# Performance work log

Measured on AMD Instinct MI355X. Metric: run time of the kernel, lower is better.

Reference implementation:

```python
import jax, jax.numpy as jnp
import numpy as np

F32 = jnp.float32
G_VEC = jnp.array([0.0, 0.0, -9.80665], dtype=F32)
# KITTI-style filter parameters (process / initial covariances)
COV_OMEGA = 1e-3; COV_ACC = 1e-2; COV_B_OMEGA = 6e-9; COV_B_ACC = 2e-4
COV_ROT_C_I = 1e-9; COV_T_C_I = 1e-9
COV_ROT0 = 1e-3; COV_V0 = 1e-1; COV_B_OMEGA0 = 1e-1; COV_B_ACC0 = 1e-1
COV_ROT_C_I0 = 1e-6; COV_T_C_I0 = 1e-5
Q_DIAG = jnp.array([COV_OMEGA]*3 + [COV_ACC]*3 + [COV_B_OMEGA]*3 + [COV_B_ACC]*3
                   + [COV_ROT_C_I]*3 + [COV_T_C_I]*3, dtype=F32)


def skew(x):
    z = jnp.zeros((), x.dtype)
    return jnp.stack([jnp.stack([z, -x[2], x[1]]),
                      jnp.stack([x[2], z, -x[0]]),
                      jnp.stack([-x[1], x[0], z])])


def so3exp(phi):
    I = jnp.eye(3, dtype=phi.dtype)
    angle = jnp.linalg.norm(phi)
    small = angle < 1e-8
    a = jnp.where(small, 1.0, angle)
    S = skew(phi)
    R = I + (jnp.sin(a) / a) * S + ((1.0 - jnp.cos(a)) / (a * a)) * (S @ S)
    return jnp.where(small, I + S, R)


def sen3exp(xi):
    phi = xi[:3]
    I = jnp.eye(3, dtype=xi.dtype)
    angle = jnp.linalg.norm(phi)
    small = angle < 1e-8
    a = jnp.where(small, 1.0, angle)
    S = skew(phi)
    SS = S @ S
    Rot = jnp.where(small, I + S,
                    I + (jnp.sin(a) / a) * S + ((1.0 - jnp.cos(a)) / (a * a)) * SS)
    J = jnp.where(small, I + 0.5 * S,
                  I + ((1.0 - jnp.cos(a)) / (a * a)) * S + ((a - jnp.sin(a)) / (a ** 3)) * SS)
    x = J @ xi[3:9].reshape(2, 3).T  # (3,2): columns dv, dp
    return Rot, x


def from_rpy(roll, pitch, yaw):
    c, s = jnp.cos, jnp.sin
    z = jnp.zeros((), roll.dtype); o = jnp.ones((), roll.dtype)
    Rz = jnp.stack([jnp.stack([c(yaw), -s(yaw), z]), jnp.stack([s(yaw), c(yaw), z]), jnp.stack([z, z, o])])
    Ry = jnp.stack([jnp.stack([c(pitch), z, s(pitch)]), jnp.stack([z, o, z]), jnp.stack([-s(pitch), z, c(pitch)])])
    Rx = jnp.stack([jnp.stack([o, z, z]), jnp.stack([z, c(roll), -s(roll)]), jnp.stack([z, s(roll), c(roll)])])
    return Rz @ Ry @ Rx


def _run(t, u, measurements_covs, v_mes, ang0, w_init):
    I3 = jnp.eye(3, dtype=F32)
    IdP = jnp.eye(21, dtype=F32)
    Q = jnp.diag(Q_DIAG)
    dt = t[1:] - t[:-1]
    # InitProcessCovNet.init_cov: beta = 10 ** tanh(W @ 1)
    beta = 10.0 ** jnp.tanh(w_init)
    P0 = jnp.zeros((21, 21), F32)
    I2 = jnp.eye(2, dtype=F32)
    P0 = P0.at[:2, :2].set(COV_ROT0 * beta[0] * I2)
    P0 = P0.at[3:5, 3:5].set(COV_V0 * beta[1] * I2)
    P0 = P0.at[9:12, 9:12].set(COV_B_OMEGA0 * beta[2] * I3)
    P0 = P0.at[12:15, 12:15].set(COV_B_ACC0 * beta[3] * I3)
    P0 = P0.at[15:18, 15:18].set(COV_ROT_C_I0 * beta[4] * I3)
    P0 = P0.at[18:21, 18:21].set(COV_T_C_I0 * beta[5] * I3)
    Rot0 = from_rpy(ang0[0], ang0[1], ang0[2])
    z3 = jnp.zeros(3, F32)
    state0 = (Rot0, v_mes[0], z3, z3, z3, I3, z3, P0)

    def step(carry, inp):
        Rot_p, v_p, p_p, bo_p, ba_p, Rci_p, tci_p, P = carry
        u_i, dt_i, mc_i = inp
        # ---- propagate ----
        acc = Rot_p @ (u_i[3:6] - ba_p) + G_VEC
        v = v_p + acc * dt_i
        p = p_p + v_p * dt_i + 0.5 * acc * dt_i * dt_i
        omega = (u_i[:3] - bo_p) * dt_i
        Rot = Rot_p @ so3exp(omega)
        # ---- covariance propagation ----
        vsr = skew(v_p) @ Rot_p
        psr = skew(p_p) @ Rot_p
        F = jnp.zeros((21, 21), F32)
        F = F.at[3:6, :3].set(skew(G_VEC))
        F = F.at[6:9, 3:6].set(I3)
        F = F.at[3:6, 12:15].set(-Rot_p)
        F = F.at[:3, 9:12].set(-Rot_p)
        F = F.at[3:6, 9:12].set(-vsr)
        F = F.at[6:9, 9:12].set(-psr)
        Gm = jnp.zeros((21, 18), F32)
        Gm = Gm.at[:3, :3].set(Rot_p)
        Gm = Gm.at[3:6, 3:6].set(Rot_p)
        Gm = Gm.at[3:6, :3].set(vsr)
        Gm = Gm.at[6:9, :3].set(psr)
        Gm = Gm.at[9:12, 6:9].set(I3)
        Gm = Gm.at[12:15, 9:12].set(I3)
        Gm = Gm.at[15:18, 12:15].set(I3)
        Gm = Gm.at[18:21, 15:18].set(I3)
        F = F * dt_i
        Gm = Gm * dt_i
        F2 = F @ F
        Phi = IdP + F + 0.5 * F2 + (F2 @ F) / 6.0
        P = Phi @ (P + Gm @ Q @ Gm.T) @ Phi.T
        # ---- update (zero lateral/vertical body velocity pseudo-measurement) ----
        Rot_body = Rot @ Rci_p
        v_imu = Rot.T @ v
        om = u_i[:3] - bo_p
        v_body = Rci_p.T @ v_imu + skew(tci_p) @ om
        Omega = skew(om)
        H_v_imu = Rci_p.T @ skew(v_imu)
        H_t = skew(tci_p)
        H = jnp.zeros((2, 21), F32)
        H = H.at[:, 3:6].set(Rot_body.T[1:])
        H = H.at[:, 15:18].set(H_v_imu[1:])
        H = H.at[:, 9:12].set(H_t[1:])
        H = H.at[:, 18:21].set(-Omega[1:])
        r = -v_body[1:]
        Rm = jnp.diag(mc_i)
        S = H @ P @ H.T + Rm
        K = jnp.linalg.solve(S, (P @ H.T).T).T  # (21,2)
        dx = K @ r
        dR, dxi = sen3exp(dx[:9])
        Rot_u = dR @ Rot
        v_u = dR @ v + dxi[:, 0]
        p_u = dR @ p + dxi[:, 1]
        bo_u = bo_p + dx[9:12]
        ba_u = ba_p + dx[12:15]
        Rci_u = so3exp(dx[15:18]) @ Rci_p
        tci_u = tci_p + dx[18:21]
        I_KH = IdP - K @ H
        P_u = I_KH @ P @ I_KH.T + K @ Rm @ K.T
        P_u = 0.5 * (P_u + P_u.T)
        new = (Rot_u, v_u, p_u, bo_u, ba_u, Rci_u, tci_u, P_u)
        return new, (Rot_u, v_u, p_u, bo_u, ba_u, Rci_u, tci_u)

    xs = (u[1:], dt, measurements_covs[1:])
    _, traj = jax.lax.scan(step, state0, xs)
    cat = lambda x0, xs_: jnp.concatenate([x0[None], xs_], axis=0)
    Rot = cat(Rot0, traj[0]); v = cat(state0[1], traj[1]); p = cat(state0[2], traj[2])
    bo = cat(state0[3], traj[3]); ba = cat(state0[4], traj[4])
    Rci = cat(I3, traj[5]); tci = cat(state0[6], traj[6])
    n = Rot.shape[0]
    # pack (Rot, v, p, b_omega, b_acc, Rot_c_i, t_c_i) -> [N, 30]
    return jnp.concatenate([Rot.reshape(n, 9), v, p, bo, ba, Rci.reshape(n, 9), tci], axis=1)


def setup_inputs() -> dict:
    key = jax.random.key(0)
    k1, k2, k3, k4, k5, k6 = jax.random.split(key, 6)
    N = 5000
    t = jnp.arange(N, dtype=F32) * 0.01  # 100 Hz IMU timestamps
    u = 0.1 * jax.random.normal(k1, (N, 6), dtype=F32)
    u = u.at[:, 5].add(9.80665)  # accel z ~ gravity
    measurements_covs = 0.5 * jax.random.uniform(k2, (N, 2), dtype=F32) + 0.1
    v_mes = jax.random.normal(k3, (N, 3), dtype=F32)
    p_mes = jax.random.normal(k4, (N, 3), dtype=F32)
    ang0 = 0.1 * jax.random.normal(k5, (3,), dtype=F32)
    w_init = 0.1 * jax.random.normal(k6, (6,), dtype=F32)
    return {"t": t, "u": u, "measurements_covs": measurements_covs,
            "v_mes": v_mes, "p_mes": p_mes, "ang0": ang0, "w_init": w_init, "N": N}


def reference(t, u, measurements_covs, v_mes, p_mes, ang0, w_init, N):
    # p_mes is accepted (as in run()) but unused: p[0] stays zero in init_run.
    return _run(t, u, measurements_covs, v_mes, ang0, w_init)
```

## Files before the change

### kernel.cpp

```cpp
#include <hip/hip_runtime.h>
#include <math.h>

#define GRV 9.80665f

__device__ __forceinline__ void so3coeffs(float a2, float* c1, float* c2, float* c3){
  if (a2 < 2.5e-3f){
    float a4 = a2*a2;
    *c1 = 1.f      - a2*(1.f/6.f)   + a4*(1.f/120.f);
    *c2 = 0.5f     - a2*(1.f/24.f)  + a4*(1.f/720.f);
    *c3 = (1.f/6.f)- a2*(1.f/120.f) + a4*(1.f/5040.f);
  } else {
    float a = sqrtf(a2);
    float sa = sinf(a), ca = cosf(a);
    *c1 = sa/a; *c2 = (1.f-ca)/a2; *c3 = (a-sa)/(a2*a);
  }
}

__device__ __forceinline__ void so3exp_u(float p0, float p1, float p2, float* R){
  float a2 = p0*p0+p1*p1+p2*p2;
  float c1,c2,c3; so3coeffs(a2,&c1,&c2,&c3);
  R[0]=1.f+c2*(p0*p0-a2); R[4]=1.f+c2*(p1*p1-a2); R[8]=1.f+c2*(p2*p2-a2);
  R[1]=-c1*p2+c2*p0*p1;   R[3]= c1*p2+c2*p0*p1;
  R[2]= c1*p1+c2*p0*p2;   R[6]=-c1*p1+c2*p0*p2;
  R[5]=-c1*p0+c2*p1*p2;   R[7]= c1*p0+c2*p1*p2;
}

__device__ __forceinline__ void mat3mul_u(const float* A, const float* B, float* C){
  #pragma unroll
  for (int r=0;r<3;r++)
    #pragma unroll
    for (int c=0;c<3;c++)
      C[r*3+c] = A[r*3]*B[c] + A[r*3+1]*B[3+c] + A[r*3+2]*B[6+c];
}

__device__ __forceinline__ void col_update(float* a, const float* R_, const float* n13,
                                           const float* n23, float dtv, float hdt2,
                                           float Gdt, float Ghdt2){
  float nb[9];
  #pragma unroll
  for (int jb=0;jb<3;jb++)
    nb[jb] = a[jb] - dtv*(R_[jb*3]*a[9]+R_[jb*3+1]*a[10]+R_[jb*3+2]*a[11]);
  #pragma unroll
  for (int r=0;r<3;r++){
    float s = a[3+r];
    if (r==0) s += Gdt*a[1];
    if (r==1) s -= Gdt*a[0];
    s += n13[r*3]*a[9]+n13[r*3+1]*a[10]+n13[r*3+2]*a[11];
    s -= dtv*(R_[r*3]*a[12]+R_[r*3+1]*a[13]+R_[r*3+2]*a[14]);
    nb[3+r]=s;
  }
  #pragma unroll
  for (int r=0;r<3;r++){
    float s = a[6+r];
    if (r==0) s += Ghdt2*a[1];
    if (r==1) s -= Ghdt2*a[0];
    s += dtv*a[3+r];
    s += n23[r*3]*a[9]+n23[r*3+1]*a[10]+n23[r*3+2]*a[11];
    s -= hdt2*(R_[r*3]*a[12]+R_[r*3+1]*a[13]+R_[r*3+2]*a[14]);
    nb[6+r]=s;
  }
  #pragma unroll
  for (int k=0;k<9;k++) a[k]=nb[k];
}

#define SEL9(e0,e1,e2,e3,e4,e5,e6,e7,e8) \
  (lane==0?(e0):lane==1?(e1):lane==2?(e2):lane==3?(e3):lane==4?(e4):lane==5?(e5):lane==6?(e6):lane==7?(e7):(e8))

__global__ __launch_bounds__(64)
void iekf_kernel(const float* __restrict__ t, const float* __restrict__ u,
                 const float* __restrict__ mcov, const float* __restrict__ vmes,
                 const float* __restrict__ ang0, const float* __restrict__ winit,
                 float* __restrict__ out, int N)
{
  const int lane = threadIdx.x;

  __shared__ float TP1[21*24];
  __shared__ float TP2[21*24];
  __shared__ float PH[44];
  __shared__ float stG[36];

  float R_[9], v_[3], p_[3], bo_[3], ba_[3], Rci_[9], tci_[3];
  float creg[21];

  float beta[6];
  #pragma unroll
  for (int k=0;k<6;k++) beta[k] = powf(10.f, tanhf(winit[k]));
  {
    float cr=cosf(ang0[0]), sr=sinf(ang0[0]);
    float cp=cosf(ang0[1]), sp=sinf(ang0[1]);
    float cy=cosf(ang0[2]), sy=sinf(ang0[2]);
    float Rz[9]={cy,-sy,0.f, sy,cy,0.f, 0.f,0.f,1.f};
    float Ry[9]={cp,0.f,sp, 0.f,1.f,0.f, -sp,0.f,cp};
    float Rx[9]={1.f,0.f,0.f, 0.f,cr,-sr, 0.f,sr,cr};
    float T1m[9]; mat3mul_u(Rz,Ry,T1m); mat3mul_u(T1m,Rx,R_);
  }
  v_[0]=vmes[0]; v_[1]=vmes[1]; v_[2]=vmes[2];
  #pragma unroll
  for (int k=0;k<3;k++){ p_[k]=0.f; bo_[k]=0.f; ba_[k]=0.f; tci_[k]=0.f; }
  #pragma unroll
  for (int k=0;k<9;k++) Rci_[k] = (k%4==0)?1.f:0.f;

  {
    float dl = (lane==0||lane==1)? 1e-3f*beta[0]
             : (lane==3||lane==4)? 0.1f*beta[1]
             : (lane>=9&&lane<12)? 0.1f*beta[2]
             : (lane>=12&&lane<15)? 0.1f*beta[3]
             : (lane>=15&&lane<18)? 1e-6f*beta[4]
             : (lane>=18&&lane<21)? 1e-5f*beta[5] : 0.f;
    #pragma unroll
    for (int j=0;j<21;j++) creg[j] = (j==lane)? dl : 0.f;
  }

  if (lane==0){
    ((float4*)stG)[0] = make_float4(R_[0],R_[1],R_[2],R_[3]);
    ((float4*)stG)[1] = make_float4(R_[4],R_[5],R_[6],R_[7]);
    ((float4*)stG)[2] = make_float4(R_[8],v_[0],v_[1],v_[2]);
    ((float4*)stG)[3] = make_float4(p_[0],p_[1],p_[2],bo_[0]);
    ((float4*)stG)[4] = make_float4(bo_[1],bo_[2],ba_[0],ba_[1]);
    ((float4*)stG)[5] = make_float4(ba_[2],Rci_[0],Rci_[1],Rci_[2]);
    ((float4*)stG)[6] = make_float4(Rci_[3],Rci_[4],Rci_[5],Rci_[6]);
    ((float4*)stG)[7] = make_float4(Rci_[7],Rci_[8],tci_[0],tci_[1]);
    ((float4*)stG)[8] = make_float4(tci_[2],0.f,0.f,0.f);
  }

  float t_nm1 = t[0];
  float t_n   = (N>1)? t[1] : t[0];
  float mc0   = (N>1)? mcov[2] : 0.f;
  float mc1   = (N>1)? mcov[3] : 0.f;
  float u6[6] = {0,0,0,0,0,0};
  if (N>1){
    #pragma unroll
    for (int k=0;k<6;k++) u6[k]=u[6+k];
  }

  for (int n=1; n<N; n++){
    const float dtv = t_n - t_nm1;
    const float dt2 = dtv*dtv;
    const float hdt2 = 0.5f*dt2;
    const float sdt3 = dt2*dtv*(1.f/6.f);
    const float Gdt = GRV*dtv;
    const float Ghdt2 = GRV*hdt2;

    if (lane<33) out[(size_t)(n-1)*33 + lane] = stG[lane];

    if (lane<21){
      float4* rp = (float4*)&TP1[lane*24];
      rp[0]=make_float4(creg[0],creg[1],creg[2],creg[3]);
      rp[1]=make_float4(creg[4],creg[5],creg[6],creg[7]);
      rp[2]=make_float4(creg[8],creg[9],creg[10],creg[11]);
      rp[3]=make_float4(creg[12],creg[13],creg[14],creg[15]);
      rp[4]=make_float4(creg[16],creg[17],creg[18],creg[19]);
      TP1[lane*24+20]=creg[20];
    }

    float vsr[9], psr[9], n13[9], n23[9];
    #pragma unroll
    for (int c=0;c<3;c++){
      vsr[c]   = v_[1]*R_[6+c] - v_[2]*R_[3+c];
      vsr[3+c] = v_[2]*R_[c]   - v_[0]*R_[6+c];
      vsr[6+c] = v_[0]*R_[3+c] - v_[1]*R_[c];
      psr[c]   = p_[1]*R_[6+c] - p_[2]*R_[3+c];
      psr[3+c] = p_[2]*R_[c]   - p_[0]*R_[6+c];
      psr[6+c] = p_[0]*R_[3+c] - p_[1]*R_[c];
    }
    #pragma unroll
    for (int c=0;c<3;c++){
      float sg0 =  GRV*R_[3+c];
      float sg1 = -GRV*R_[c];
      n13[c]   = -dtv*vsr[c]   - hdt2*sg0;
      n13[3+c] = -dtv*vsr[3+c] - hdt2*sg1;
      n13[6+c] = -dtv*vsr[6+c];
      n23[c]   = -dtv*psr[c]   - hdt2*vsr[c]   - sdt3*sg0;
      n23[3+c] = -dtv*psr[3+c] - hdt2*vsr[3+c] - sdt3*sg1;
      n23[6+c] = -dtv*psr[6+c] - hdt2*vsr[6+c];
    }

    float Rn[9], vnp[3], pnp[3];
    {
      float ub0=u6[3]-ba_[0], ub1=u6[4]-ba_[1], ub2=u6[5]-ba_[2];
      float ac0=R_[0]*ub0+R_[1]*ub1+R_[2]*ub2;
      float ac1=R_[3]*ub0+R_[4]*ub1+R_[5]*ub2;
      float ac2=R_[6]*ub0+R_[7]*ub1+R_[8]*ub2 - GRV;
      vnp[0]=v_[0]+ac0*dtv; vnp[1]=v_[1]+ac1*dtv; vnp[2]=v_[2]+ac2*dtv;
      pnp[0]=p_[0]+v_[0]*dtv+0.5f*ac0*dt2;
      pnp[1]=p_[1]+v_[1]*dtv+0.5f*ac1*dt2;
      pnp[2]=p_[2]+v_[2]*dtv+0.5f*ac2*dt2;
      float E[9]; so3exp_u((u6[0]-bo_[0])*dtv,(u6[1]-bo_[1])*dtv,(u6[2]-bo_[2])*dtv, E);
      mat3mul_u(R_, E, Rn);
    }
    float Hc0[21], Hc1[21], rsh0, rsh1;
    {
      float Rb[9]; mat3mul_u(Rn, Rci_, Rb);
      float vi0 = Rn[0]*vnp[0]+Rn[3]*vnp[1]+Rn[6]*vnp[2];
      float vi1 = Rn[1]*vnp[0]+Rn[4]*vnp[1]+Rn[7]*vnp[2];
      float vi2 = Rn[2]*vnp[0]+Rn[5]*vnp[1]+Rn[8]*vnp[2];
      float o0 = u6[0]-bo_[0], o1 = u6[1]-bo_[1], o2 = u6[2]-bo_[2];
      #pragma unroll
      for (int c=0;c<3;c++){ Hc0[c]=0.f; Hc1[c]=0.f; Hc0[6+c]=0.f; Hc1[6+c]=0.f; Hc0[12+c]=0.f; Hc1[12+c]=0.f; }
      #pragma unroll
      for (int c=0;c<3;c++){ Hc0[3+c]=Rb[c*3+1]; Hc1[3+c]=Rb[c*3+2]; }
      Hc0[9]= tci_[2]; Hc0[10]=0.f;      Hc0[11]=-tci_[0];
      Hc1[9]=-tci_[1]; Hc1[10]=tci_[0];  Hc1[11]=0.f;
      Hc0[15]= Rci_[4]*vi2 - Rci_[7]*vi1;
      Hc0[16]=-Rci_[1]*vi2 + Rci_[7]*vi0;
      Hc0[17]= Rci_[1]*vi1 - Rci_[4]*vi0;
      Hc1[15]= Rci_[5]*vi2 - Rci_[8]*vi1;
      Hc1[16]=-Rci_[2]*vi2 + Rci_[8]*vi0;
      Hc1[17]= Rci_[2]*vi1 - Rci_[5]*vi0;
      Hc0[18]=-o2; Hc0[19]=0.f; Hc0[20]= o0;
      Hc1[18]= o1; Hc1[19]=-o0; Hc1[20]=0.f;
      rsh0 = -( Rci_[1]*vi0 + Rci_[4]*vi1 + Rci_[7]*vi2 + (tci_[2]*o0 - tci_[0]*o2) );
      rsh1 = -( Rci_[2]*vi0 + Rci_[5]*vi1 + Rci_[8]*vi2 + (-tci_[1]*o0 + tci_[0]*o1) );
    }

    float areg[21];
    if (lane<21){
      float colv[21];
      #pragma unroll
      for (int r=0;r<21;r++) colv[r] = TP1[r*24+lane];
      #pragma unroll
      for (int j=0;j<21;j++) areg[j] = 0.5f*(creg[j]+colv[j]);
    } else {
      #pragma unroll
      for (int j=0;j<21;j++) areg[j] = 0.f;
    }
    {
      const float qom = 1e-3f*dt2, qac = 1e-2f*dt2;
      if (lane<9){
        float wi0 = SEL9(R_[0],R_[3],R_[6], vsr[0],vsr[3],vsr[6], psr[0],psr[3],psr[6]);
        float wi1 = SEL9(R_[1],R_[4],R_[7], vsr[1],vsr[4],vsr[7], psr[1],psr[4],psr[7]);
        float wi2 = SEL9(R_[2],R_[5],R_[8], vsr[2],vsr[5],vsr[8], psr[2],psr[5],psr[8]);
        #pragma unroll
        for (int jq=0;jq<9;jq++){
          float wj0 = (jq<3)? R_[jq*3]   : (jq<6)? vsr[(jq-3)*3]   : psr[(jq-6)*3];
          float wj1 = (jq<3)? R_[jq*3+1] : (jq<6)? vsr[(jq-3)*3+1] : psr[(jq-6)*3+1];
          float wj2 = (jq<3)? R_[jq*3+2] : (jq<6)? vsr[(jq-3)*3+2] : psr[(jq-6)*3+2];
          areg[jq] += qom*(wi0*wj0+wi1*wj1+wi2*wj2);
        }
        if (lane>=3 && lane<6){
          float ri0 = (lane==3)?R_[0]:(lane==4)?R_[3]:R_[6];
          float ri1 = (lane==3)?R_[1]:(lane==4)?R_[4]:R_[7];
          float ri2 = (lane==3)?R_[2]:(lane==4)?R_[5]:R_[8];
          areg[3] += qac*(ri0*R_[0]+ri1*R_[1]+ri2*R_[2]);
          areg[4] += qac*(ri0*R_[3]+ri1*R_[4]+ri2*R_[5]);
          areg[5] += qac*(ri0*R_[6]+ri1*R_[7]+ri2*R_[8]);
        }
      }
      float qd = (lane>=9&&lane<12)? 6e-9f : (lane>=12&&lane<15)? 2e-4f : (lane>=15&&lane<21)? 1e-9f : 0.f;
      qd *= dt2;
      #pragma unroll
      for (int j=9;j<21;j++) if (j==lane) areg[j] += qd;
    }

    col_update(areg, R_, n13, n23, dtv, hdt2, Gdt, Ghdt2);

    if (lane<21){
      float4* rp = (float4*)&TP2[lane*24];
      rp[0]=make_float4(areg[0],areg[1],areg[2],areg[3]);
      rp[1]=make_float4(areg[4],areg[5],areg[6],areg[7]);
      rp[2]=make_float4(areg[8],areg[9],areg[10],areg[11]);
      rp[3]=make_float4(areg[12],areg[13],areg[14],areg[15]);
      rp[4]=make_float4(areg[16],areg[17],areg[18],areg[19]);
      TP2[lane*24+20]=areg[20];
    }
    float ctreg[21];
    if (lane<21){
      #pragma unroll
      for (int r=0;r<21;r++) ctreg[r] = TP2[r*24+lane];
    } else {
      #pragma unroll
      for (int r=0;r<21;r++) ctreg[r] = 0.f;
    }

    col_update(ctreg, R_, n13, n23, dtv, hdt2, Gdt, Ghdt2);

    float ph0=0.f, ph1=0.f;
    #pragma unroll
    for (int j=0;j<21;j++){ ph0 += ctreg[j]*Hc0[j]; ph1 += ctreg[j]*Hc1[j]; }
    if (lane<21){
      *(float2*)&PH[lane*2] = make_float2(ph0, ph1);
    }
    float pj0[21], pj1[21];
    {
      #pragma unroll
      for (int q=0;q<11;q++){
        float4 v4 = ((float4*)PH)[q];
        if (2*q   < 21){ pj0[2*q]   = v4.x; pj1[2*q]   = v4.y; }
        if (2*q+1 < 21){ pj0[2*q+1] = v4.z; pj1[2*q+1] = v4.w; }
      }
    }

    float s00=mc0, s01=0.f, s10=0.f, s11=mc1;
    #pragma unroll
    for (int j=0;j<21;j++){
      s00 += Hc0[j]*pj0[j];
      s01 += Hc0[j]*pj1[j];
      s10 += Hc1[j]*pj0[j];
      s11 += Hc1[j]*pj1[j];
    }
    float id  = 1.f/(s00*s11 - s01*s10);
    float i00 =  s11*id, i01 = -s01*id, i10 = -s10*id, i11 = s00*id;
    float sm01 = 0.5f*(s01+s10);
    float dx[21];
    #pragma unroll
    for (int j=0;j<21;j++){
      float kj0 = pj0[j]*i00 + pj1[j]*i10;
      float kj1 = pj0[j]*i01 + pj1[j]*i11;
      dx[j] = kj0*rsh0 + kj1*rsh1;
    }

    {
      float q0=dx[0], q1=dx[1], q2=dx[2];
      float a2 = q0*q0+q1*q1+q2*q2;
      float c1,c2,c3; so3coeffs(a2,&c1,&c2,&c3);
      float dR[9], Jm[9];
      dR[0]=1.f+c2*(q0*q0-a2); dR[4]=1.f+c2*(q1*q1-a2); dR[8]=1.f+c2*(q2*q2-a2);
      dR[1]=-c1*q2+c2*q0*q1;   dR[3]= c1*q2+c2*q0*q1;
      dR[2]= c1*q1+c2*q0*q2;   dR[6]=-c1*q1+c2*q0*q2;
      dR[5]=-c1*q0+c2*q1*q2;   dR[7]= c1*q0+c2*q1*q2;
      Jm[0]=1.f+c3*(q0*q0-a2); Jm[4]=1.f+c3*(q1*q1-a2); Jm[8]=1.f+c3*(q2*q2-a2);
      Jm[1]=-c2*q2+c3*q0*q1;   Jm[3]= c2*q2+c3*q0*q1;
      Jm[2]= c2*q1+c3*q0*q2;   Jm[6]=-c2*q1+c3*q0*q2;
      Jm[5]=-c2*q0+c3*q1*q2;   Jm[7]= c2*q0+c3*q1*q2;
      float xv[3], xp[3];
      #pragma unroll
      for (int r=0;r<3;r++){
        xv[r]=Jm[r*3]*dx[3]+Jm[r*3+1]*dx[4]+Jm[r*3+2]*dx[5];
        xp[r]=Jm[r*3]*dx[6]+Jm[r*3+1]*dx[7]+Jm[r*3+2]*dx[8];
      }
      float Rn2[9]; mat3mul_u(dR, Rn, Rn2);
      #pragma unroll
      for (int r=0;r<3;r++){
        float vv = dR[r*3]*vnp[0]+dR[r*3+1]*vnp[1]+dR[r*3+2]*vnp[2] + xv[r];
        float pp = dR[r*3]*pnp[0]+dR[r*3+1]*pnp[1]+dR[r*3+2]*pnp[2] + xp[r];
        v_[r]=vv; p_[r]=pp;
        bo_[r]+=dx[9+r]; ba_[r]+=dx[12+r]; tci_[r]+=dx[18+r];
      }
      float E2[9]; so3exp_u(dx[15],dx[16],dx[17],E2);
      float Rc2[9]; mat3mul_u(E2, Rci_, Rc2);
      #pragma unroll
      for (int k=0;k<9;k++){ Rci_[k]=Rc2[k]; R_[k]=Rn2[k]; }
    }
    if (lane==0){
      ((float4*)stG)[0] = make_float4(R_[0],R_[1],R_[2],R_[3]);
      ((float4*)stG)[1] = make_float4(R_[4],R_[5],R_[6],R_[7]);
      ((float4*)stG)[2] = make_float4(R_[8],v_[0],v_[1],v_[2]);
      ((float4*)stG)[3] = make_float4(p_[0],p_[1],p_[2],bo_[0]);
      ((float4*)stG)[4] = make_float4(bo_[1],bo_[2],ba_[0],ba_[1]);
      ((float4*)stG)[5] = make_float4(ba_[2],Rci_[0],Rci_[1],Rci_[2]);
      ((float4*)stG)[6] = make_float4(Rci_[3],Rci_[4],Rci_[5],Rci_[6]);
      ((float4*)stG)[7] = make_float4(Rci_[7],Rci_[8],tci_[0],tci_[1]);
      ((float4*)stG)[8] = make_float4(tci_[2],0.f,0.f,0.f);
    }

    {
      float ki0 = ph0*i00 + ph1*i10;
      float ki1 = ph0*i01 + ph1*i11;
      float ai0 = s00*ki0 + sm01*ki1;
      float ai1 = sm01*ki0 + s11*ki1;
      #pragma unroll
      for (int j=0;j<21;j++){
        float kj0 = pj0[j]*i00 + pj1[j]*i10;
        float kj1 = pj0[j]*i01 + pj1[j]*i11;
        float tsum = (ki0*pj0[j] + ki1*pj1[j]) + (ph0*kj0 + ph1*kj1);
        float quad = ai0*kj0 + ai1*kj1;
        creg[j] = ctreg[j] - tsum + quad;
      }
    }

    {
      int np = n+1;
      t_nm1 = t_n;
      if (np < N){
        t_n = t[np];
        mc0 = mcov[np*2]; mc1 = mcov[np*2+1];
        #pragma unroll
        for (int k=0;k<6;k++) u6[k]=u[np*6+k];
      }
    }
  }

  if (lane<33) out[(size_t)(N-1)*33 + lane] = stG[lane];
}

extern "C" void kernel_launch(void* const* d_in, const int* in_sizes, int n_in,
                              void* d_out, int out_size, void* d_ws, size_t ws_size,
                              hipStream_t stream) {
  const float* t     = (const float*)d_in[0];
  const float* u     = (const float*)d_in[1];
  const float* mcov  = (const float*)d_in[2];
  const float* vmes  = (const float*)d_in[3];
  const float* ang0  = (const float*)d_in[5];
  const float* winit = (const float*)d_in[6];
  float* out = (float*)d_out;
  int N = in_sizes[0];
  iekf_kernel<<<dim3(1), dim3(64), 0, stream>>>(t, u, mcov, vmes, ang0, winit, out, N);
}
```

Baseline: 15.28 ms.

## Restructure IEKF step: sparse H, closed-form Q term, reordered covariance update, prefetch

Replaces dense 21-wide H vectors with explicit nonzero entries. Computes the process-noise term from the skew structure instead of generic 9x9 products, and reorders the covariance propagation so the P·H^T product is taken from the half-updated matrix before the second column update. The Kalman correction becomes a rank-2 update with precomputed scalars. Input loads are double-buffered one extra step ahead to hide global memory latency on this serial, latency-bound loop. These changes alter floating-point summation order and add register pressure.

Measured after the change: 18.67 ms. +22.1%, slower.

```diff
diff --git a/kernel.cpp b/kernel.cpp
--- a/kernel.cpp
+++ b/kernel.cpp
@@ -63,9 +63,6 @@
   for (int k=0;k<9;k++) a[k]=nb[k];
 }
 
-#define SEL9(e0,e1,e2,e3,e4,e5,e6,e7,e8) \
-  (lane==0?(e0):lane==1?(e1):lane==2?(e2):lane==3?(e3):lane==4?(e4):lane==5?(e5):lane==6?(e6):lane==7?(e7):(e8))
-
 __global__ __launch_bounds__(64)
 void iekf_kernel(const float* __restrict__ t, const float* __restrict__ u,
                  const float* __restrict__ mcov, const float* __restrict__ vmes,
@@ -125,12 +122,19 @@
 
   float t_nm1 = t[0];
   float t_n   = (N>1)? t[1] : t[0];
+  float t_np  = (N>2)? t[2] : t_n;
   float mc0   = (N>1)? mcov[2] : 0.f;
   float mc1   = (N>1)? mcov[3] : 0.f;
-  float u6[6] = {0,0,0,0,0,0};
+  float mc0b  = (N>2)? mcov[4] : 0.f;
+  float mc1b  = (N>2)? mcov[5] : 0.f;
+  float u6[6] = {0,0,0,0,0,0}, u6b[6] = {0,0,0,0,0,0};
   if (N>1){
     #pragma unroll
     for (int k=0;k<6;k++) u6[k]=u[6+k];
+  }
+  if (N>2){
+    #pragma unroll
+    for (int k=0;k<6;k++) u6b[k]=u[12+k];
   }
 
   for (int n=1; n<N; n++){
@@ -174,6 +178,9 @@
       n23[3+c] = -dtv*psr[3+c] - hdt2*vsr[3+c] - sdt3*sg1;
       n23[6+c] = -dtv*psr[6+c] - hdt2*vsr[6+c];
     }
+    const float vv = v_[0]*v_[0]+v_[1]*v_[1]+v_[2]*v_[2];
+    const float vp = v_[0]*p_[0]+v_[1]*p_[1]+v_[2]*p_[2];
+    const float pp = p_[0]*p_[0]+p_[1]*p_[1]+p_[2]*p_[2];
 
     float Rn[9], vnp[3], pnp[3];
     {
@@ -188,38 +195,35 @@
       float E[9]; so3exp_u((u6[0]-bo_[0])*dtv,(u6[1]-bo_[1])*dtv,(u6[2]-bo_[2])*dtv, E);
       mat3mul_u(R_, E, Rn);
     }
-    float Hc0[21], Hc1[21], rsh0, rsh1;
+    float h0_3,h0_4,h0_5,h0_9,h0_11,h0_15,h0_16,h0_17,h0_18,h0_20;
+    float h1_3,h1_4,h1_5,h1_9,h1_10,h1_15,h1_16,h1_17,h1_18,h1_19;
+    float rsh0, rsh1;
     {
       float Rb[9]; mat3mul_u(Rn, Rci_, Rb);
       float vi0 = Rn[0]*vnp[0]+Rn[3]*vnp[1]+Rn[6]*vnp[2];
       float vi1 = Rn[1]*vnp[0]+Rn[4]*vnp[1]+Rn[7]*vnp[2];
       float vi2 = Rn[2]*vnp[0]+Rn[5]*vnp[1]+Rn[8]*vnp[2];
       float o0 = u6[0]-bo_[0], o1 = u6[1]-bo_[1], o2 = u6[2]-bo_[2];
-      #pragma unroll
-      for (int c=0;c<3;c++){ Hc0[c]=0.f; Hc1[c]=0.f; Hc0[6+c]=0.f; Hc1[6+c]=0.f; Hc0[12+c]=0.f; Hc1[12+c]=0.f; }
-      #pragma unroll
-      for (int c=0;c<3;c++){ Hc0[3+c]=Rb[c*3+1]; Hc1[3+c]=Rb[c*3+2]; }
-      Hc0[9]= tci_[2]; Hc0[10]=0.f;      Hc0[11]=-tci_[0];
-      Hc1[9]=-tci_[1]; Hc1[10]=tci_[0];  Hc1[11]=0.f;
-      Hc0[15]= Rci_[4]*vi2 - Rci_[7]*vi1;
-      Hc0[16]=-Rci_[1]*vi2 + Rci_[7]*vi0;
-      Hc0[17]= Rci_[1]*vi1 - Rci_[4]*vi0;
-      Hc1[15]= Rci_[5]*vi2 - Rci_[8]*vi1;
-      Hc1[16]=-Rci_[2]*vi2 + Rci_[8]*vi0;
-      Hc1[17]= Rci_[2]*vi1 - Rci_[5]*vi0;
-      Hc0[18]=-o2; Hc0[19]=0.f; Hc0[20]= o0;
-      Hc1[18]= o1; Hc1[19]=-o0; Hc1[20]=0.f;
+      h0_3 = Rb[1]; h0_4 = Rb[4]; h0_5 = Rb[7];
+      h1_3 = Rb[2]; h1_4 = Rb[5]; h1_5 = Rb[8];
+      h0_9 = tci_[2];  h0_11 = -tci_[0];
+      h1_9 = -tci_[1]; h1_10 = tci_[0];
+      h0_15 =  Rci_[4]*vi2 - Rci_[7]*vi1;
+      h0_16 = -Rci_[1]*vi2 + Rci_[7]*vi0;
+      h0_17 =  Rci_[1]*vi1 - Rci_[4]*vi0;
+      h1_15 =  Rci_[5]*vi2 - Rci_[8]*vi1;
+      h1_16 = -Rci_[2]*vi2 + Rci_[8]*vi0;
+      h1_17 =  Rci_[2]*vi1 - Rci_[5]*vi0;
+      h0_18 = -o2; h0_20 = o0;
+      h1_18 =  o1; h1_19 = -o0;
       rsh0 = -( Rci_[1]*vi0 + Rci_[4]*vi1 + Rci_[7]*vi2 + (tci_[2]*o0 - tci_[0]*o2) );
       rsh1 = -( Rci_[2]*vi0 + Rci_[5]*vi1 + Rci_[8]*vi2 + (-tci_[1]*o0 + tci_[0]*o1) );
     }
 
     float areg[21];
     if (lane<21){
-      float colv[21];
-      #pragma unroll
-      for (int r=0;r<21;r++) colv[r] = TP1[r*24+lane];
-      #pragma unroll
-      for (int j=0;j<21;j++) areg[j] = 0.5f*(creg[j]+colv[j]);
+      #pragma unroll
+      for (int j=0;j<21;j++) areg[j] = 0.5f*(creg[j] + TP1[j*24+lane]);
     } else {
       #pragma unroll
       for (int j=0;j<21;j++) areg[j] = 0.f;
@@ -227,32 +231,47 @@
     {
       const float qom = 1e-3f*dt2, qac = 1e-2f*dt2;
       if (lane<9){
-        float wi0 = SEL9(R_[0],R_[3],R_[6], vsr[0],vsr[3],vsr[6], psr[0],psr[3],psr[6]);
-        float wi1 = SEL9(R_[1],R_[4],R_[7], vsr[1],vsr[4],vsr[7], psr[1],psr[4],psr[7]);
-        float wi2 = SEL9(R_[2],R_[5],R_[8], vsr[2],vsr[5],vsr[8], psr[2],psr[5],psr[8]);
-        #pragma unroll
-        for (int jq=0;jq<9;jq++){
-          float wj0 = (jq<3)? R_[jq*3]   : (jq<6)? vsr[(jq-3)*3]   : psr[(jq-6)*3];
-          float wj1 = (jq<3)? R_[jq*3+1] : (jq<6)? vsr[(jq-3)*3+1] : psr[(jq-6)*3+1];
-          float wj2 = (jq<3)? R_[jq*3+2] : (jq<6)? vsr[(jq-3)*3+2] : psr[(jq-6)*3+2];
-          areg[jq] += qom*(wi0*wj0+wi1*wj1+wi2*wj2);
+        int bi = lane/3, r3 = lane - 3*bi;
+        float vrr = (r3==0)?v_[0]:(r3==1)?v_[1]:v_[2];
+        float prr = (r3==0)?p_[0]:(r3==1)?p_[1]:p_[2];
+        float sv0 = (r3==0)?0.f:(r3==1)? v_[2]:-v_[1];
+        float sv1 = (r3==0)?-v_[2]:(r3==1)?0.f: v_[0];
+        float sv2 = (r3==0)? v_[1]:(r3==1)?-v_[0]:0.f;
+        float sp0 = (r3==0)?0.f:(r3==1)? p_[2]:-p_[1];
+        float sp1 = (r3==0)?-p_[2]:(r3==1)?0.f: p_[0];
+        float sp2 = (r3==0)? p_[1]:(r3==1)?-p_[0]:0.f;
+        if (bi==0){
+          areg[r3]  += qom;
+          areg[3] -= qom*sv0; areg[4] -= qom*sv1; areg[5] -= qom*sv2;
+          areg[6] -= qom*sp0; areg[7] -= qom*sp1; areg[8] -= qom*sp2;
+        } else if (bi==1){
+          areg[0] += qom*sv0; areg[1] += qom*sv1; areg[2] += qom*sv2;
+          areg[3+r3] += qom*vv + qac;
+          areg[3] -= qom*vrr*v_[0]; areg[4] -= qom*vrr*v_[1]; areg[5] -= qom*vrr*v_[2];
+          areg[6+r3] += qom*vp;
+          areg[6] -= qom*prr*v_[0]; areg[7] -= qom*prr*v_[1]; areg[8] -= qom*prr*v_[2];
+        } else {
+          areg[0] += qom*sp0; areg[1] += qom*sp1; areg[2] += qom*sp2;
+          areg[3+r3] += qom*vp;
+          areg[3] -= qom*vrr*p_[0]; areg[4] -= qom*vrr*p_[1]; areg[5] -= qom*vrr*p_[2];
+          areg[6+r3] += qom*pp;
+          areg[6] -= qom*prr*p_[0]; areg[7] -= qom*prr*p_[1]; areg[8] -= qom*prr*p_[2];
         }
-        if (lane>=3 && lane<6){
-          float ri0 = (lane==3)?R_[0]:(lane==4)?R_[3]:R_[6];
-          float ri1 = (lane==3)?R_[1]:(lane==4)?R_[4]:R_[7];
-          float ri2 = (lane==3)?R_[2]:(lane==4)?R_[5]:R_[8];
-          areg[3] += qac*(ri0*R_[0]+ri1*R_[1]+ri2*R_[2]);
-          areg[4] += qac*(ri0*R_[3]+ri1*R_[4]+ri2*R_[5]);
-          areg[5] += qac*(ri0*R_[6]+ri1*R_[7]+ri2*R_[8]);
-        }
+      } else if (lane<21){
+        float qd = (lane<12)? 6e-9f : (lane<15)? 2e-4f : 1e-9f;
+        areg[lane] += qd*dt2;
       }
-      float qd = (lane>=9&&lane<12)? 6e-9f : (lane>=12&&lane<15)? 2e-4f : (lane>=15&&lane<21)? 1e-9f : 0.f;
-      qd *= dt2;
-      #pragma unroll
-      for (int j=9;j<21;j++) if (j==lane) areg[j] += qd;
     }
 
     col_update(areg, R_, n13, n23, dtv, hdt2, Gdt, Ghdt2);
+
+    float y0 = (((areg[3]*h0_3 + areg[4]*h0_4) + (areg[5]*h0_5 + areg[9]*h0_9)) +
+                ((areg[11]*h0_11 + areg[15]*h0_15) + (areg[16]*h0_16 + areg[17]*h0_17))) +
+               (areg[18]*h0_18 + areg[20]*h0_20);
+    float y1 = (((areg[3]*h1_3 + areg[4]*h1_4) + (areg[5]*h1_5 + areg[9]*h1_9)) +
+                ((areg[10]*h1_10 + areg[15]*h1_15) + (areg[16]*h1_16 + areg[17]*h1_17))) +
+               (areg[18]*h1_18 + areg[19]*h1_19);
+    if (lane<21) *(float2*)&PH[lane*2] = make_float2(y0, y1);
 
     if (lane<21){
       float4* rp = (float4*)&TP2[lane*24];
@@ -263,6 +282,16 @@
       rp[4]=make_float4(areg[16],areg[17],areg[18],areg[19]);
       TP2[lane*24+20]=areg[20];
     }
+
+    float y0v[21], y1v[21];
+    {
+      #pragma unroll
+      for (int q=0;q<11;q++){
+        float4 v4 = ((float4*)PH)[q];
+        if (2*q   < 21){ y0v[2*q]   = v4.x; y1v[2*q]   = v4.y; }
+        if (2*q+1 < 21){ y0v[2*q+1] = v4.z; y1v[2*q+1] = v4.w; }
+      }
+    }
     float ctreg[21];
     if (lane<21){
       #pragma unroll
@@ -272,41 +301,48 @@
       for (int r=0;r<21;r++) ctreg[r] = 0.f;
     }
 
-    col_update(ctreg, R_, n13, n23, dtv, hdt2, Gdt, Ghdt2);
-
-    float ph0=0.f, ph1=0.f;
-    #pragma unroll
-    for (int j=0;j<21;j++){ ph0 += ctreg[j]*Hc0[j]; ph1 += ctreg[j]*Hc1[j]; }
-    if (lane<21){
-      *(float2*)&PH[lane*2] = make_float2(ph0, ph1);
-    }
-    float pj0[21], pj1[21];
-    {
-      #pragma unroll
-      for (int q=0;q<11;q++){
-        float4 v4 = ((float4*)PH)[q];
-        if (2*q   < 21){ pj0[2*q]   = v4.x; pj1[2*q]   = v4.y; }
-        if (2*q+1 < 21){ pj0[2*q+1] = v4.z; pj1[2*q+1] = v4.w; }
-      }
-    }
-
-    float s00=mc0, s01=0.f, s10=0.f, s11=mc1;
-    #pragma unroll
-    for (int j=0;j<21;j++){
-      s00 += Hc0[j]*pj0[j];
-      s01 += Hc0[j]*pj1[j];
-      s10 += Hc1[j]*pj0[j];
-      s11 += Hc1[j]*pj1[j];
-    }
+    col_update(y0v, R_, n13, n23, dtv, hdt2, Gdt, Ghdt2);
+    col_update(y1v, R_, n13, n23, dtv, hdt2, Gdt, Ghdt2);
+
+    float s00 = mc0 + ((((h0_3*y0v[3] + h0_4*y0v[4]) + (h0_5*y0v[5] + h0_9*y0v[9])) +
+                        ((h0_11*y0v[11] + h0_15*y0v[15]) + (h0_16*y0v[16] + h0_17*y0v[17]))) +
+                       (h0_18*y0v[18] + h0_20*y0v[20]));
+    float s01 =        ((((h0_3*y1v[3] + h0_4*y1v[4]) + (h0_5*y1v[5] + h0_9*y1v[9])) +
+                        ((h0_11*y1v[11] + h0_15*y1v[15]) + (h0_16*y1v[16] + h0_17*y1v[17]))) +
+                       (h0_18*y1v[18] + h0_20*y1v[20]));
+    float s10 =        ((((h1_3*y0v[3] + h1_4*y0v[4]) + (h1_5*y0v[5] + h1_9*y0v[9])) +
+                        ((h1_10*y0v[10] + h1_15*y0v[15]) + (h1_16*y0v[16] + h1_17*y0v[17]))) +
+                       (h1_18*y0v[18] + h1_19*y0v[19]));
+    float s11 = mc1 + ((((h1_3*y1v[3] + h1_4*y1v[4]) + (h1_5*y1v[5] + h1_9*y1v[9])) +
+                        ((h1_10*y1v[10] + h1_15*y1v[15]) + (h1_16*y1v[16] + h1_17*y1v[17]))) +
+                       (h1_18*y1v[18] + h1_19*y1v[19]));
     float id  = 1.f/(s00*s11 - s01*s10);
     float i00 =  s11*id, i01 = -s01*id, i10 = -s10*id, i11 = s00*id;
     float sm01 = 0.5f*(s01+s10);
+    float g0 = i00*rsh0 + i01*rsh1;
+    float g1 = i10*rsh0 + i11*rsh1;
+
     float dx[21];
     #pragma unroll
-    for (int j=0;j<21;j++){
-      float kj0 = pj0[j]*i00 + pj1[j]*i10;
-      float kj1 = pj0[j]*i01 + pj1[j]*i11;
-      dx[j] = kj0*rsh0 + kj1*rsh1;
+    for (int j=0;j<21;j++) dx[j] = y0v[j]*g0 + y1v[j]*g1;
+
+    col_update(ctreg, R_, n13, n23, dtv, hdt2, Gdt, Ghdt2);
+
+    {
+      float ph0 = (((ctreg[3]*h0_3 + ctreg[4]*h0_4) + (ctreg[5]*h0_5 + ctreg[9]*h0_9)) +
+                   ((ctreg[11]*h0_11 + ctreg[15]*h0_15) + (ctreg[16]*h0_16 + ctreg[17]*h0_17))) +
+                  (ctreg[18]*h0_18 + ctreg[20]*h0_20);
+      float ph1 = (((ctreg[3]*h1_3 + ctreg[4]*h1_4) + (ctreg[5]*h1_5 + ctreg[9]*h1_9)) +
+                   ((ctreg[10]*h1_10 + ctreg[15]*h1_15) + (ctreg[16]*h1_16 + ctreg[17]*h1_17))) +
+                  (ctreg[18]*h1_18 + ctreg[19]*h1_19);
+      float ki0 = ph0*i00 + ph1*i10;
+      float ki1 = ph0*i01 + ph1*i11;
+      float ai0 = s00*ki0 + sm01*ki1;
+      float ai1 = sm01*ki0 + s11*ki1;
+      float al = -ki0 + (ai0 - ph0)*i00 + (ai1 - ph1)*i01;
+      float be = -ki1 + (ai0 - ph0)*i10 + (ai1 - ph1)*i11;
+      #pragma unroll
+      for (int j=0;j<21;j++) creg[j] = ctreg[j] + al*y0v[j] + be*y1v[j];
     }
 
     {
@@ -331,9 +367,9 @@
       float Rn2[9]; mat3mul_u(dR, Rn, Rn2);
       #pragma unroll
       for (int r=0;r<3;r++){
-        float vv = dR[r*3]*vnp[0]+dR[r*3+1]*vnp[1]+dR[r*3+2]*vnp[2] + xv[r];
-        float pp = dR[r*3]*pnp[0]+dR[r*3+1]*pnp[1]+dR[r*3+2]*pnp[2] + xp[r];
-        v_[r]=vv; p_[r]=pp;
+        float vv2 = dR[r*3]*vnp[0]+dR[r*3+1]*vnp[1]+dR[r*3+2]*vnp[2] + xv[r];
+        float pp2 = dR[r*3]*pnp[0]+dR[r*3+1]*pnp[1]+dR[r*3+2]*pnp[2] + xp[r];
+        v_[r]=vv2; p_[r]=pp2;
         bo_[r]+=dx[9+r]; ba_[r]+=dx[12+r]; tci_[r]+=dx[18+r];
       }
       float E2[9]; so3exp_u(dx[15],dx[16],dx[17],E2);
@@ -354,28 +390,16 @@
     }
 
     {
-      float ki0 = ph0*i00 + ph1*i10;
-      float ki1 = ph0*i01 + ph1*i11;
-      float ai0 = s00*ki0 + sm01*ki1;
-      float ai1 = sm01*ki0 + s11*ki1;
-      #pragma unroll
-      for (int j=0;j<21;j++){
-        float kj0 = pj0[j]*i00 + pj1[j]*i10;
-        float kj1 = pj0[j]*i01 + pj1[j]*i11;
-        float tsum = (ki0*pj0[j] + ki1*pj1[j]) + (ph0*kj0 + ph1*kj1);
-        float quad = ai0*kj0 + ai1*kj1;
-        creg[j] = ctreg[j] - tsum + quad;
-      }
-    }
-
-    {
-      int np = n+1;
-      t_nm1 = t_n;
-      if (np < N){
-        t_n = t[np];
-        mc0 = mcov[np*2]; mc1 = mcov[np*2+1];
+      t_nm1 = t_n; t_n = t_np;
+      mc0 = mc0b; mc1 = mc1b;
+      #pragma unroll
+      for (int k=0;k<6;k++) u6[k]=u6b[k];
+      int np2 = n+2;
+      if (np2 < N){
+        t_np = t[np2];
+        mc0b = mcov[np2*2]; mc1b = mcov[np2*2+1];
         #pragma unroll
-        for (int k=0;k<6;k++) u6[k]=u[np*6+k];
+        for (int k=0;k<6;k++) u6b[k]=u[np2*6+k];
       }
     }
   }
```
